# Kernel optimization log

Hardware: AMD Instinct MI355X
Metric: run time of the kernel (lower is better)

Reference implementation:

```python
import jax, jax.numpy as jnp
import numpy as np

N = 50000      # nodes
E = 800000     # edges (before self-loops)
DIN = 256      # in_channel
H = 1          # heads (PyG GATConv default)
C = 128        # out_channel per head
NEG_SLOPE = 0.2


def setup_inputs() -> dict:
    key = jax.random.key(0)
    k1, k2, k3, k4, k5 = jax.random.split(key, 5)
    x = jax.random.normal(k1, (N, DIN), jnp.float32)
    # random edges guaranteed to have no self-loops (PyG removes then re-adds them)
    src = jax.random.randint(k2, (E,), 0, N, dtype=jnp.int32)
    off = jax.random.randint(k3, (E,), 1, N, dtype=jnp.int32)
    dst = (src + off) % N
    edge_index = jnp.stack([src, dst])  # [2, E], row0=source j, row1=target i
    W = jax.random.normal(k4, (DIN, H * C), jnp.float32) / np.sqrt(DIN)
    att = jax.random.normal(k5, (1, H, 2 * C), jnp.float32) * 0.1
    bias = jnp.zeros((H * C,), jnp.float32)
    return {"x": x, "edge_index": edge_index, "W": W, "att": att, "bias": bias}


def reference(x, edge_index, W, att, bias):
    n = x.shape[0]
    h = (x @ W).reshape(n, H, C)                       # [N,H,C]
    # add self-loops (PyG GATConv forward)
    loops = jnp.arange(n, dtype=edge_index.dtype)
    src = jnp.concatenate([edge_index[0], loops])       # [Et]
    dst = jnp.concatenate([edge_index[1], loops])       # [Et]
    h_i = h[dst]                                        # [Et,H,C] target feats
    h_j = h[src]                                        # [Et,H,C] source feats
    # per-edge attention logit: sum(cat(x_i, x_j) * att)
    alpha = jnp.sum(jnp.concatenate([h_i, h_j], axis=-1) * att, axis=-1)  # [Et,H]
    alpha = jax.nn.leaky_relu(alpha, NEG_SLOPE)
    # segment softmax grouped by destination node (numerically stable)
    amax = jax.ops.segment_max(alpha, dst, num_segments=n)  # [N,H]
    ex = jnp.exp(alpha - amax[dst])
    denom = jax.ops.segment_sum(ex, dst, num_segments=n)    # [N,H]
    a = ex / (denom[dst] + 1e-16)                            # [Et,H]
    # scatter-aggregate weighted source features to targets
    out = jax.ops.segment_sum(h_j * a[..., None], dst, num_segments=n)  # [N,H,C]
    return out.reshape(n, H * C) + bias
```

## Files before the change

### kernel.cpp

```cpp
#include <hip/hip_runtime.h>
#include <hip/hip_bf16.h>

constexpr int N_NODES = 50000;
constexpr int DIN     = 256;
constexpr int C_OUT   = 128;
constexpr int E_EDGES = 800000;
constexpr int ET      = E_EDGES + N_NODES;
constexpr float NEG_SLOPE = 0.2f;

constexpr int NHI      = 196;
constexpr int CAP      = 6144;
constexpr int PEPC     = 8192;
constexpr int NPB_PART = (ET + PEPC - 1) / PEPC;
constexpr int GEMM_RPB    = 64;
constexpr int GEMM_BLOCKS = (N_NODES + GEMM_RPB - 1) / GEMM_RPB;
constexpr int AGG_NPB     = 32;
constexpr int AGG_BLOCKS  = (N_NODES + AGG_NPB - 1) / AGG_NPB;

typedef __attribute__((ext_vector_type(8))) short short8v;
typedef __attribute__((ext_vector_type(4))) float f32x4;

static __device__ __forceinline__ ushort f2bf(float f) {
    __hip_bfloat16 b = __float2bfloat16(f);
    return *reinterpret_cast<ushort*>(&b);
}
static __device__ __forceinline__ short f2bfs(float f) {
    __hip_bfloat16 b = __float2bfloat16(f);
    return *reinterpret_cast<short*>(&b);
}

__global__ __launch_bounds__(256) void wconv_kernel(const float* __restrict__ W,
                                                    ushort* __restrict__ wt,
                                                    int* __restrict__ gcur) {
    const int t = threadIdx.x;
    const int idx = blockIdx.x * 256 + t;
    if (idx < DIN * C_OUT) {
        const int k = idx >> 7, col = idx & 127;
        const int ks = k >> 5, kgrp = (k >> 3) & 3, j = k & 7;
        const int cc = col >> 4, col16 = col & 15;
        wt[((ks * 8 + cc) * 64 + kgrp * 16 + col16) * 8 + j] = f2bf(W[idx]);
    }
    if (blockIdx.x == 0 && t < NHI) gcur[t] = 0;
}

__global__ __launch_bounds__(256) void part_gemm(const float* __restrict__ x,
                                                 const ushort* __restrict__ wt,
                                                 const float* __restrict__ att,
                                                 const int* __restrict__ ei,
                                                 ushort* __restrict__ hb,
                                                 float* __restrict__ s_dst,
                                                 float* __restrict__ s_src,
                                                 int* __restrict__ gcur,
                                                 int2* __restrict__ ebuf) {
    __shared__ ushort lw[DIN * C_OUT / 2];
    const int t = threadIdx.x;

    if (blockIdx.x < NPB_PART) {
        int* li    = (int*)lw;
        int* hist  = li;
        int* basel = li + 256;
        int* curl  = li + 512;
        const int c = blockIdx.x;
        hist[t] = 0;
        __syncthreads();
        #pragma unroll 4
        for (int i = 0; i < 32; i++) {
            const int e = c * PEPC + i * 256 + t;
            if (e < ET) {
                const int d = (e < E_EDGES) ? ei[E_EDGES + e] : (e - E_EDGES);
                atomicAdd(&hist[d >> 8], 1);
            }
        }
        __syncthreads();
        if (t < NHI) basel[t] = atomicAdd(&gcur[t], hist[t]);
        curl[t] = 0;
        __syncthreads();
        #pragma unroll 4
        for (int i = 0; i < 32; i++) {
            const int e = c * PEPC + i * 256 + t;
            if (e < ET) {
                int s, d;
                if (e < E_EDGES) { s = ei[e]; d = ei[E_EDGES + e]; }
                else             { s = e - E_EDGES; d = s; }
                const int hi = d >> 8;
                const int r = atomicAdd(&curl[hi], 1);
                const int pos = basel[hi] + r;
                if (pos < CAP) ebuf[(size_t)hi * CAP + pos] = make_int2(s, d);
            }
        }
        return;
    }

    const int gb = blockIdx.x - NPB_PART;
    const int lane = t & 63, wv = t >> 6;
    const int col16 = lane & 15, kgrp = lane >> 4;
    const int rowbase = gb * GEMM_RPB + wv * 16;
    int r0 = rowbase + col16; if (r0 >= N_NODES) r0 = N_NODES - 1;
    const float* xr0 = x + (size_t)r0 * DIN + kgrp * 8;

    f32x4 acc[8] = {};
    const short8v* lwf = (const short8v*)lw;
    #pragma unroll
    for (int ph = 0; ph < 2; ph++) {
        if (ph) __syncthreads();
        {
            const uint4* src = (const uint4*)(wt + ph * (DIN * C_OUT / 2));
            uint4* dst = (uint4*)lw;
            #pragma unroll
            for (int i = 0; i < 8; i++) dst[t + i * 256] = src[t + i * 256];
        }
        short8v A0[4];
        #pragma unroll
        for (int ks = 0; ks < 4; ks++) {
            const int kg = ph * 4 + ks;
            const float4 v0 = *(const float4*)(xr0 + kg * 32);
            const float4 v1 = *(const float4*)(xr0 + kg * 32 + 4);
            short8v a;
            a[0] = f2bfs(v0.x); a[1] = f2bfs(v0.y); a[2] = f2bfs(v0.z); a[3] = f2bfs(v0.w);
            a[4] = f2bfs(v1.x); a[5] = f2bfs(v1.y); a[6] = f2bfs(v1.z); a[7] = f2bfs(v1.w);
            A0[ks] = a;
        }
        __syncthreads();
        #pragma unroll
        for (int ks = 0; ks < 4; ks++) {
            #pragma unroll
            for (int c = 0; c < 8; c++) {
                const short8v bfr = lwf[(ks * 8 + c) * 64 + lane];
                acc[c] = __builtin_amdgcn_mfma_f32_16x16x32_bf16(A0[ks], bfr, acc[c], 0, 0, 0);
            }
        }
    }

    float attd[8], atts[8];
    #pragma unroll
    for (int c = 0; c < 8; c++) {
        attd[c] = att[c * 16 + col16];
        atts[c] = att[C_OUT + c * 16 + col16];
    }
    #pragma unroll
    for (int j = 0; j < 4; j++) {
        const int row = rowbase + kgrp * 4 + j;
        const bool ok = (row < N_NODES);
        float pd = 0.f, ps = 0.f;
        #pragma unroll
        for (int c = 0; c < 8; c++) {
            const float hv = acc[c][j];
            pd += hv * attd[c];
            ps += hv * atts[c];
            if (ok) hb[(size_t)row * C_OUT + c * 16 + col16] = f2bf(hv);
        }
        #pragma unroll
        for (int off = 1; off < 16; off <<= 1) {
            pd += __shfl_xor(pd, off);
            ps += __shfl_xor(ps, off);
        }
        if (col16 == 0 && ok) { s_dst[row] = pd; s_src[row] = ps; }
    }
}

__global__ __launch_bounds__(256) void final_kernel(const int* __restrict__ gcur,
                                                    const int2* __restrict__ ebuf,
                                                    int2* __restrict__ offs2,
                                                    int* __restrict__ esrc) {
    __shared__ int histl[256], sA[256], sE[256], curl[256];
    const int t = threadIdx.x, hi = blockIdx.x;
    const int n = min(gcur[hi], CAP);
    const size_t segbase = (size_t)hi * CAP;
    histl[t] = 0;
    __syncthreads();
    for (int k = t; k < n; k += 256)
        atomicAdd(&histl[ebuf[segbase + k].y & 255], 1);
    __syncthreads();
    const int v = histl[t];
    sA[t] = v;
    __syncthreads();
    #pragma unroll
    for (int off = 1; off < 256; off <<= 1) {
        const int y = (t >= off) ? sA[t - off] : 0;
        __syncthreads();
        sA[t] += y;
        __syncthreads();
    }
    sE[t] = sA[t] - v;
    curl[t] = 0;
    const int node = hi * 256 + t;
    if (node < N_NODES) {
        const int beg = (int)segbase + sE[t];
        offs2[node] = make_int2(beg, beg + v);
    }
    __syncthreads();
    for (int k = t; k < n; k += 256) {
        const int2 e2 = ebuf[segbase + k];
        const int lo = e2.y & 255;
        const int r = atomicAdd(&curl[lo], 1);
        esrc[segbase + sE[lo] + r] = e2.x;
    }
}

__global__ __launch_bounds__(256) void aggregate_kernel(
    const ushort* __restrict__ hb, const int2* __restrict__ offs2,
    const int* __restrict__ esrc, const float* __restrict__ s_dst,
    const float* __restrict__ s_src, const float* __restrict__ bias,
    float* __restrict__ out) {
    const int t = threadIdx.x;
    const int wv = t >> 6, lane = t & 63;
    const int sub = lane >> 3, l8 = lane & 7;
    const int node = blockIdx.x * AGG_NPB + wv * 8 + sub;
    const bool valid = (node < N_NODES);

    const int2 be = valid ? offs2[node] : make_int2(0, 0);
    const float sd = valid ? s_dst[node] : 0.f;
    float den = 0.f;
    float acc[16] = {};
    const uint4* __restrict__ h4 = (const uint4*)hb;

    for (int e = be.x; e < be.y; e++) {
        const int s = esrc[e];
        float a = sd + s_src[s];
        a = (a > 0.f) ? a : NEG_SLOPE * a;
        const float w = __expf(a);
        den += w;
        const uint4 hv0 = h4[(size_t)s * 16 + l8];
        const uint4 hv1 = h4[(size_t)s * 16 + 8 + l8];
        acc[0]  += w * __uint_as_float(hv0.x << 16);
        acc[1]  += w * __uint_as_float(hv0.x & 0xffff0000u);
        acc[2]  += w * __uint_as_float(hv0.y << 16);
        acc[3]  += w * __uint_as_float(hv0.y & 0xffff0000u);
        acc[4]  += w * __uint_as_float(hv0.z << 16);
        acc[5]  += w * __uint_as_float(hv0.z & 0xffff0000u);
        acc[6]  += w * __uint_as_float(hv0.w << 16);
        acc[7]  += w * __uint_as_float(hv0.w & 0xffff0000u);
        acc[8]  += w * __uint_as_float(hv1.x << 16);
        acc[9]  += w * __uint_as_float(hv1.x & 0xffff0000u);
        acc[10] += w * __uint_as_float(hv1.y << 16);
        acc[11] += w * __uint_as_float(hv1.y & 0xffff0000u);
        acc[12] += w * __uint_as_float(hv1.z << 16);
        acc[13] += w * __uint_as_float(hv1.z & 0xffff0000u);
        acc[14] += w * __uint_as_float(hv1.w << 16);
        acc[15] += w * __uint_as_float(hv1.w & 0xffff0000u);
    }
    if (!valid) return;
    const float inv = 1.f / (den + 1e-16f);
    float* op = out + (size_t)node * C_OUT;
    #pragma unroll
    for (int half = 0; half < 2; half++) {
        const int base = half * 64 + l8 * 8;
        const float4 b0 = *(const float4*)(bias + base);
        const float4 b1 = *(const float4*)(bias + base + 4);
        float4 o0 = make_float4(acc[half * 8 + 0] * inv + b0.x, acc[half * 8 + 1] * inv + b0.y,
                                acc[half * 8 + 2] * inv + b0.z, acc[half * 8 + 3] * inv + b0.w);
        float4 o1 = make_float4(acc[half * 8 + 4] * inv + b1.x, acc[half * 8 + 5] * inv + b1.y,
                                acc[half * 8 + 6] * inv + b1.z, acc[half * 8 + 7] * inv + b1.w);
        *(float4*)(op + base)     = o0;
        *(float4*)(op + base + 4) = o1;
    }
}

extern "C" void kernel_launch(void* const* d_in, const int* in_sizes, int n_in,
                              void* d_out, int out_size, void* d_ws, size_t ws_size,
                              hipStream_t stream) {
    const float* x    = (const float*)d_in[0];
    const int*   ei   = (const int*)d_in[1];
    const float* W    = (const float*)d_in[2];
    const float* att  = (const float*)d_in[3];
    const float* bias = (const float*)d_in[4];
    float* out = (float*)d_out;

    ushort* wt    = (ushort*)d_ws;
    ushort* hbuf  = wt + DIN * C_OUT;
    int2*   ebuf  = (int2*)(hbuf + (size_t)N_NODES * C_OUT);
    int*    esrc  = (int*)(ebuf + (size_t)NHI * CAP);
    float*  s_src = (float*)(esrc + (size_t)NHI * CAP);
    float*  s_dst = s_src + N_NODES;
    int2*   offs2 = (int2*)(s_dst + N_NODES);
    int*    gcur  = (int*)(offs2 + N_NODES);

    wconv_kernel<<<(DIN * C_OUT + 255) / 256, 256, 0, stream>>>(W, wt, gcur);
    part_gemm<<<NPB_PART + GEMM_BLOCKS, 256, 0, stream>>>(
        x, wt, att, ei, hbuf, s_dst, s_src, gcur, ebuf);
    final_kernel<<<NHI, 256, 0, stream>>>(gcur, ebuf, offs2, esrc);
    aggregate_kernel<<<AGG_BLOCKS, 256, 0, stream>>>(
        hbuf, offs2, esrc, s_dst, s_src, bias, out);
}
```

Measured before the change: 91.07 us.

## Regroup partition with weight conversion, pack edge records, transpose MFMA output

Edge partitioning now runs in the same launch as the W-to-bf16 conversion, and the GEMM becomes its own kernel, so GEMM blocks no longer share a grid with partition blocks. The gcur counters are cleared with a memset. Edge buffer entries shrink from int2 to a single packed int holding the low 8 bits of dst and a 16-bit source, halving the scatter traffic. MFMA operands are swapped so each lane holds four consecutive columns, which allows packed 8-byte bf16 stores and a shorter shuffle reduction for the attention scores. The 16-bit source packing only holds while N is at most 65536, which 50000 meets.

```diff
diff --git a/kernel.cpp b/kernel.cpp
--- a/kernel.cpp
+++ b/kernel.cpp
@@ -12,6 +12,7 @@
 constexpr int CAP      = 6144;
 constexpr int PEPC     = 8192;
 constexpr int NPB_PART = (ET + PEPC - 1) / PEPC;
+constexpr int WCONV_BLOCKS = (DIN * C_OUT) / 256;
 constexpr int GEMM_RPB    = 64;
 constexpr int GEMM_BLOCKS = (N_NODES + GEMM_RPB - 1) / GEMM_RPB;
 constexpr int AGG_NPB     = 32;
@@ -29,37 +30,14 @@
     return *reinterpret_cast<short*>(&b);
 }
 
-__global__ __launch_bounds__(256) void wconv_kernel(const float* __restrict__ W,
-                                                    ushort* __restrict__ wt,
-                                                    int* __restrict__ gcur) {
+__global__ __launch_bounds__(256) void part_wconv(const float* __restrict__ W,
+                                                  const int* __restrict__ ei,
+                                                  ushort* __restrict__ wt,
+                                                  int* __restrict__ gcur,
+                                                  int* __restrict__ ebuf) {
     const int t = threadIdx.x;
-    const int idx = blockIdx.x * 256 + t;
-    if (idx < DIN * C_OUT) {
-        const int k = idx >> 7, col = idx & 127;
-        const int ks = k >> 5, kgrp = (k >> 3) & 3, j = k & 7;
-        const int cc = col >> 4, col16 = col & 15;
-        wt[((ks * 8 + cc) * 64 + kgrp * 16 + col16) * 8 + j] = f2bf(W[idx]);
-    }
-    if (blockIdx.x == 0 && t < NHI) gcur[t] = 0;
-}
-
-__global__ __launch_bounds__(256) void part_gemm(const float* __restrict__ x,
-                                                 const ushort* __restrict__ wt,
-                                                 const float* __restrict__ att,
-                                                 const int* __restrict__ ei,
-                                                 ushort* __restrict__ hb,
-                                                 float* __restrict__ s_dst,
-                                                 float* __restrict__ s_src,
-                                                 int* __restrict__ gcur,
-                                                 int2* __restrict__ ebuf) {
-    __shared__ ushort lw[DIN * C_OUT / 2];
-    const int t = threadIdx.x;
-
     if (blockIdx.x < NPB_PART) {
-        int* li    = (int*)lw;
-        int* hist  = li;
-        int* basel = li + 256;
-        int* curl  = li + 512;
+        __shared__ int hist[256], basel[256], curl[256];
         const int c = blockIdx.x;
         hist[t] = 0;
         __syncthreads();
@@ -85,17 +63,33 @@
                 const int hi = d >> 8;
                 const int r = atomicAdd(&curl[hi], 1);
                 const int pos = basel[hi] + r;
-                if (pos < CAP) ebuf[(size_t)hi * CAP + pos] = make_int2(s, d);
+                if (pos < CAP) ebuf[(size_t)hi * CAP + pos] = ((d & 255) << 16) | s;
             }
         }
         return;
     }
-
-    const int gb = blockIdx.x - NPB_PART;
+    const int idx = (blockIdx.x - NPB_PART) * 256 + t;
+    if (idx < DIN * C_OUT) {
+        const int k = idx >> 7, col = idx & 127;
+        const int ks = k >> 5, kgrp = (k >> 3) & 3, j = k & 7;
+        const int cc = col >> 4, col16 = col & 15;
+        wt[((ks * 8 + cc) * 64 + kgrp * 16 + col16) * 8 + j] = f2bf(W[idx]);
+    }
+}
+
+__global__ __launch_bounds__(256) void gemm_mfma(const float* __restrict__ x,
+                                                 const ushort* __restrict__ wt,
+                                                 const float* __restrict__ att,
+                                                 ushort* __restrict__ hb,
+                                                 float* __restrict__ s_dst,
+                                                 float* __restrict__ s_src) {
+    __shared__ ushort lw[DIN * C_OUT / 2];
+    const int t = threadIdx.x;
     const int lane = t & 63, wv = t >> 6;
     const int col16 = lane & 15, kgrp = lane >> 4;
-    const int rowbase = gb * GEMM_RPB + wv * 16;
-    int r0 = rowbase + col16; if (r0 >= N_NODES) r0 = N_NODES - 1;
+    const int rowbase = blockIdx.x * GEMM_RPB + wv * 16;
+    const int hrow = rowbase + col16;
+    int r0 = hrow; if (r0 >= N_NODES) r0 = N_NODES - 1;
     const float* xr0 = x + (size_t)r0 * DIN + kgrp * 8;
 
     f32x4 acc[8] = {};
@@ -126,40 +120,34 @@
             #pragma unroll
             for (int c = 0; c < 8; c++) {
                 const short8v bfr = lwf[(ks * 8 + c) * 64 + lane];
-                acc[c] = __builtin_amdgcn_mfma_f32_16x16x32_bf16(A0[ks], bfr, acc[c], 0, 0, 0);
+                acc[c] = __builtin_amdgcn_mfma_f32_16x16x32_bf16(bfr, A0[ks], acc[c], 0, 0, 0);
             }
         }
     }
 
-    float attd[8], atts[8];
+    const bool ok = (hrow < N_NODES);
+    float pd = 0.f, ps = 0.f;
     #pragma unroll
     for (int c = 0; c < 8; c++) {
-        attd[c] = att[c * 16 + col16];
-        atts[c] = att[C_OUT + c * 16 + col16];
-    }
-    #pragma unroll
-    for (int j = 0; j < 4; j++) {
-        const int row = rowbase + kgrp * 4 + j;
-        const bool ok = (row < N_NODES);
-        float pd = 0.f, ps = 0.f;
-        #pragma unroll
-        for (int c = 0; c < 8; c++) {
-            const float hv = acc[c][j];
-            pd += hv * attd[c];
-            ps += hv * atts[c];
-            if (ok) hb[(size_t)row * C_OUT + c * 16 + col16] = f2bf(hv);
-        }
-        #pragma unroll
-        for (int off = 1; off < 16; off <<= 1) {
-            pd += __shfl_xor(pd, off);
-            ps += __shfl_xor(ps, off);
-        }
-        if (col16 == 0 && ok) { s_dst[row] = pd; s_src[row] = ps; }
-    }
+        const int colb = c * 16 + kgrp * 4;
+        const float4 ad = *(const float4*)(att + colb);
+        const float4 as = *(const float4*)(att + C_OUT + colb);
+        pd += acc[c][0] * ad.x + acc[c][1] * ad.y + acc[c][2] * ad.z + acc[c][3] * ad.w;
+        ps += acc[c][0] * as.x + acc[c][1] * as.y + acc[c][2] * as.z + acc[c][3] * as.w;
+        if (ok) {
+            uint2 pk;
+            pk.x = (uint)(ushort)f2bf(acc[c][0]) | ((uint)(ushort)f2bf(acc[c][1]) << 16);
+            pk.y = (uint)(ushort)f2bf(acc[c][2]) | ((uint)(ushort)f2bf(acc[c][3]) << 16);
+            *(uint2*)(hb + (size_t)hrow * C_OUT + colb) = pk;
+        }
+    }
+    pd += __shfl_xor(pd, 16); pd += __shfl_xor(pd, 32);
+    ps += __shfl_xor(ps, 16); ps += __shfl_xor(ps, 32);
+    if (kgrp == 0 && ok) { s_dst[hrow] = pd; s_src[hrow] = ps; }
 }
 
 __global__ __launch_bounds__(256) void final_kernel(const int* __restrict__ gcur,
-                                                    const int2* __restrict__ ebuf,
+                                                    const int* __restrict__ ebuf,
                                                     int2* __restrict__ offs2,
                                                     int* __restrict__ esrc) {
     __shared__ int histl[256], sA[256], sE[256], curl[256];
@@ -169,7 +157,7 @@
     histl[t] = 0;
     __syncthreads();
     for (int k = t; k < n; k += 256)
-        atomicAdd(&histl[ebuf[segbase + k].y & 255], 1);
+        atomicAdd(&histl[(ebuf[segbase + k] >> 16) & 255], 1);
     __syncthreads();
     const int v = histl[t];
     sA[t] = v;
@@ -190,10 +178,10 @@
     }
     __syncthreads();
     for (int k = t; k < n; k += 256) {
-        const int2 e2 = ebuf[segbase + k];
-        const int lo = e2.y & 255;
+        const int e2 = ebuf[segbase + k];
+        const int lo = (e2 >> 16) & 255;
         const int r = atomicAdd(&curl[lo], 1);
-        esrc[segbase + sE[lo] + r] = e2.x;
+        esrc[segbase + sE[lo] + r] = e2 & 0xFFFF;
     }
 }
 
@@ -268,16 +256,16 @@
 
     ushort* wt    = (ushort*)d_ws;
     ushort* hbuf  = wt + DIN * C_OUT;
-    int2*   ebuf  = (int2*)(hbuf + (size_t)N_NODES * C_OUT);
-    int*    esrc  = (int*)(ebuf + (size_t)NHI * CAP);
+    int*    ebuf  = (int*)(hbuf + (size_t)N_NODES * C_OUT);
+    int*    esrc  = ebuf + (size_t)NHI * CAP;
     float*  s_src = (float*)(esrc + (size_t)NHI * CAP);
     float*  s_dst = s_src + N_NODES;
     int2*   offs2 = (int2*)(s_dst + N_NODES);
     int*    gcur  = (int*)(offs2 + N_NODES);
 
-    wconv_kernel<<<(DIN * C_OUT + 255) / 256, 256, 0, stream>>>(W, wt, gcur);
-    part_gemm<<<NPB_PART + GEMM_BLOCKS, 256, 0, stream>>>(
-        x, wt, att, ei, hbuf, s_dst, s_src, gcur, ebuf);
+    hipMemsetAsync(gcur, 0, NHI * sizeof(int), stream);
+    part_wconv<<<NPB_PART + WCONV_BLOCKS, 256, 0, stream>>>(W, ei, wt, gcur, ebuf);
+    gemm_mfma<<<GEMM_BLOCKS, 256, 0, stream>>>(x, wt, att, hbuf, s_dst, s_src);
     final_kernel<<<NHI, 256, 0, stream>>>(gcur, ebuf, offs2, esrc);
     aggregate_kernel<<<AGG_BLOCKS, 256, 0, stream>>>(
         hbuf, offs2, esrc, s_dst, s_src, bias, out);
```

Measured after the change: 101.4 us. 1.11x slower.
